# Kernel optimization log

Measured on AMD Instinct MI355X. Metric: run time of the kernel, lower is better.

The kernel has to match this reference:

```python
import jax, jax.numpy as jnp
import numpy as np

B, S, D = 2, 2048, 768          # batch, n_ctx, d_model
NQK, DQK = 12, 64               # n_qk_heads, d_qk_head
NOV, DOV = 768, 1               # n_ov_heads, d_ov_head
R = NOV // NQK                  # OV heads per QK head
VKV = 4                         # virtual_kv_num
BASE = 10000.0
SCALE = DQK ** 0.5              # cfg.attn_scale default


def _rotary_sin_cos():
    # TransformerLens-style (non-adjacent-pairs): freq repeated as (2 d)
    pos = jnp.arange(S, dtype=jnp.float32)
    freq = BASE ** (jnp.arange(0, DQK, 2, dtype=jnp.float32) / DQK)
    freq = jnp.concatenate([freq, freq])          # [DQK]
    angles = pos[:, None] / freq[None, :]         # [S, DQK]
    return jnp.sin(angles), jnp.cos(angles)


def _apply_rotary(x, sin, cos):
    # x: [b, pos, head, DQK]; rotary_dim == d_qk_head so full rotation
    half = DQK // 2
    rot = jnp.concatenate([-x[..., half:], x[..., :half]], axis=-1)
    return x * cos[None, :, None, :] + rot * sin[None, :, None, :]


def setup_inputs() -> dict:
    key = jax.random.key(0)
    ks = jax.random.split(key, 7)
    std_qk = (2.0 / (D * DQK)) ** 0.5   # kaiming fan_in (d_model*d_head)
    std_ov = (2.0 / (D * DOV)) ** 0.5
    std_o = (2.0 / (DOV * D)) ** 0.5
    sin, cos = _rotary_sin_cos()
    return {
        "resid": jax.random.normal(ks[0], (B, S, D), jnp.float32),
        "W_Q": jax.random.normal(ks[1], (NQK, D, DQK), jnp.float32) * std_qk,
        "W_K": jax.random.normal(ks[2], (NQK, D, DQK), jnp.float32) * std_qk,
        "W_V": jax.random.normal(ks[3], (NOV, D, DOV), jnp.float32) * std_ov,
        "W_O": jax.random.normal(ks[4], (NOV, DOV, D), jnp.float32) * std_o,
        "b_Q": jnp.zeros((NQK, DQK), jnp.float32),
        "b_K": jnp.zeros((NQK, DQK), jnp.float32),
        "b_V": jnp.zeros((NOV, DOV), jnp.float32),
        "virtual_k": jax.random.normal(ks[5], (VKV, NQK, DQK), jnp.float32) * (2.0 / (NQK * DQK)) ** 0.5,
        "virtual_v": jnp.zeros((VKV, NOV, DOV), jnp.float32),  # init zeros, requires_grad=False
        "rotary_sin": sin,
        "rotary_cos": cos,
    }


def reference(resid, W_Q, W_K, W_V, W_O, b_Q, b_K, b_V,
              virtual_k, virtual_v, rotary_sin, rotary_cos):
    # q/k/v projections: per-head low-rank maps + bias  -> [b, s, h, d]
    q = jnp.einsum('bsm,hmd->bshd', resid, W_Q) + b_Q
    k = jnp.einsum('bsm,hmd->bshd', resid, W_K) + b_K
    v = jnp.einsum('bsm,hmd->bshd', resid, W_V) + b_V
    # rotary on q and k
    q = _apply_rotary(q, rotary_sin, rotary_cos)
    k = _apply_rotary(k, rotary_sin, rotary_cos)
    # append virtual KV tokens at the end of the key axis
    k = jnp.concatenate([k, jnp.broadcast_to(virtual_k[None], (B, VKV, NQK, DQK))], axis=1)
    v = jnp.concatenate([v, jnp.broadcast_to(virtual_v[None], (B, VKV, NOV, DOV))], axis=1)
    # full attention scores [b, nqk, S, S+VKV]
    scores = jnp.einsum('bqhd,bkhd->bhqk', q, k) / SCALE
    # causal mask: tril(ones(S, S+VKV), diagonal=VKV) -> key j visible iff j <= i + VKV
    qi = jnp.arange(S)[:, None]
    kj = jnp.arange(S + VKV)[None, :]
    mask = kj <= qi + VKV
    scores = jnp.where(mask[None, None], scores, -jnp.inf)
    pattern = jax.nn.softmax(scores, axis=-1)
    pattern = jnp.where(jnp.isnan(pattern), 0.0, pattern)
    # group OV heads by QK head: v [b, k, NOV, DOV] -> [b, NQK, R, k, DOV]
    v_r = jnp.transpose(v, (0, 2, 1, 3)).reshape(B, NQK, R, S + VKV, DOV)
    z = jnp.einsum('bnqk,bnrkh->bnrqh', pattern, v_r)       # [b, NQK, R, S, DOV]
    z = z.reshape(B, NOV, S, DOV).transpose(0, 2, 1, 3)      # [b, S, NOV, DOV]
    out = jnp.einsum('bqhd,hdm->bqm', z, W_O)                # cal_out (no b_O)
    return out
```

## Files before the change

### kernel.cpp

```cpp
#include <hip/hip_runtime.h>

typedef __attribute__((ext_vector_type(8))) __bf16 bf16x8;
typedef __attribute__((ext_vector_type(4))) __bf16 bf16x4;
typedef __attribute__((ext_vector_type(4))) float  f32x4;

__device__ __forceinline__ void gld_lds16(const void* g, void* l) {
  __builtin_amdgcn_global_load_lds(
      (const __attribute__((address_space(1))) unsigned int*)g,
      (__attribute__((address_space(3))) unsigned int*)l, 16, 0, 0);
}


__global__ __launch_bounds__(256) void prep_kernel(
    const float* __restrict__ resid, const float* __restrict__ WQ,
    const float* __restrict__ WK, const float* __restrict__ WV,
    const float* __restrict__ WO,
    __bf16* __restrict__ Rb, __bf16* __restrict__ Wt1, __bf16* __restrict__ Wt2)
{
  int t = blockIdx.x * 256 + threadIdx.x;
  if (t < 786432) {
    f32x4 v = *(const f32x4*)(resid + (size_t)t * 4);
    bf16x4 o;
#pragma unroll
    for (int j = 0; j < 4; ++j) o[j] = (__bf16)v[j];
    *(bf16x4*)(Rb + (size_t)t * 4) = o;
    return;
  }
  t -= 786432;
  if (t < 1769472) {
    int nn = t / 768, k = t - nn * 768;
    float v;
    if (nn < 768)       v = WQ[(nn >> 6) * 49152 + k * 64 + (nn & 63)];
    else if (nn < 1536) v = WK[((nn - 768) >> 6) * 49152 + k * 64 + ((nn - 768) & 63)];
    else                v = WV[(nn - 1536) * 768 + k];
    Wt1[t] = (__bf16)v;
    return;
  }
  t -= 1769472;
  int nn = t / 768, k = t - nn * 768;
  Wt2[t] = (__bf16)WO[k * 768 + nn];
}

template<int OUTF>
__global__ __launch_bounds__(256) void gemm_bt(
    const __bf16* __restrict__ A, const __bf16* __restrict__ Bt,
    void* __restrict__ C, int M, int N, int K, int ldc)
{
  __shared__ __align__(16) char smem[65536];
  const int tid = threadIdx.x;
  const int l = tid & 63, wv = tid >> 6;
  const int wr = wv >> 1, wc = wv & 1;
  const int l15 = l & 15, lg = l >> 4;
  const int m0 = blockIdx.y * 128, n0 = blockIdx.x * 128;
  const int sw = (l15 & 7) << 4;

  auto stage = [&](int buf, int k0) {
    char* a_l = smem + buf * 32768;
    char* b_l = a_l + 16384;
#pragma unroll
    for (int c = 0; c < 4; ++c) {
      int i2 = c * 256 + tid;
      int row = i2 >> 3, slt = i2 & 7;
      gld_lds16(A + (size_t)(m0 + row) * K + k0 + ((slt ^ (row & 7)) * 8), a_l + i2 * 16);
    }
#pragma unroll
    for (int c = 0; c < 4; ++c) {
      int i2 = c * 256 + tid;
      int row = i2 >> 3, slt = i2 & 7;
      gld_lds16(Bt + (size_t)(n0 + row) * K + k0 + ((slt ^ (row & 7)) * 8), b_l + i2 * 16);
    }
  };

  f32x4 acc[4][4] = {};
  stage(0, 0);
  __syncthreads();
  int cur = 0;
  for (int k0 = 0; k0 < K; k0 += 64) {
    if (k0 + 64 < K) stage(cur ^ 1, k0 + 64);
    char* a_lds = smem + cur * 32768;
    char* b_lds = a_lds + 16384;
#pragma unroll
    for (int kk = 0; kk < 2; ++kk) {
      bf16x8 af[4], bfr[4];
#pragma unroll
      for (int i = 0; i < 4; ++i) {
        int mr = wr * 64 + i * 16 + l15;
        af[i]  = *(const bf16x8*)(a_lds + mr * 128 + ((lg * 16 + kk * 64) ^ sw));
        int nr = wc * 64 + i * 16 + l15;
        bfr[i] = *(const bf16x8*)(b_lds + nr * 128 + ((lg * 16 + kk * 64) ^ sw));
      }
#pragma unroll
      for (int i = 0; i < 4; ++i)
#pragma unroll
        for (int j = 0; j < 4; ++j)
          acc[i][j] = __builtin_amdgcn_mfma_f32_16x16x32_bf16(af[i], bfr[j], acc[i][j], 0, 0, 0);
    }
    __syncthreads();
    cur ^= 1;
  }
#pragma unroll
  for (int i = 0; i < 4; ++i)
#pragma unroll
    for (int j = 0; j < 4; ++j)
#pragma unroll
      for (int r = 0; r < 4; ++r) {
        int row = m0 + wr * 64 + i * 16 + lg * 4 + r;
        int col = n0 + wc * 64 + j * 16 + l15;
        if (OUTF) ((float*)C)[(size_t)row * ldc + col] = acc[i][j][r];
        else      ((__bf16*)C)[(size_t)row * ldc + col] = (__bf16)acc[i][j][r];
      }
}

__global__ __launch_bounds__(256) void qk_rotary(
    const __bf16* __restrict__ qkv, const float* __restrict__ bQ,
    const float* __restrict__ bK, const float* __restrict__ vk,
    const float* __restrict__ rsin, const float* __restrict__ rcos,
    __bf16* __restrict__ Qb, __bf16* __restrict__ Kb)
{
  int t = blockIdx.x * 256 + threadIdx.x;
  if (t < 196608) {
    int d0 = (t & 3) * 8;
    int x = t >> 2;
    int bh = x >> 11, s = x & 2047;
    int b = bh / 12, h = bh - b * 12;
    const __bf16* rowp = qkv + ((size_t)(b * 2048 + s)) * 2304 + h * 64;
    bf16x8 ql = *(const bf16x8*)(rowp + d0);
    bf16x8 qu = *(const bf16x8*)(rowp + d0 + 32);
    bf16x8 kl = *(const bf16x8*)(rowp + 768 + d0);
    bf16x8 ku = *(const bf16x8*)(rowp + 768 + d0 + 32);
    const float* bql = bQ + h * 64 + d0;
    const float* bkl = bK + h * 64 + d0;
    const float* snp = rsin + s * 64 + d0;
    const float* csp = rcos + s * 64 + d0;
    f32x4 bq0 = *(const f32x4*)(bql),      bq1 = *(const f32x4*)(bql + 4);
    f32x4 bq2 = *(const f32x4*)(bql + 32), bq3 = *(const f32x4*)(bql + 36);
    f32x4 bk0 = *(const f32x4*)(bkl),      bk1 = *(const f32x4*)(bkl + 4);
    f32x4 bk2 = *(const f32x4*)(bkl + 32), bk3 = *(const f32x4*)(bkl + 36);
    f32x4 sl0 = *(const f32x4*)(snp),      sl1 = *(const f32x4*)(snp + 4);
    f32x4 su0 = *(const f32x4*)(snp + 32), su1 = *(const f32x4*)(snp + 36);
    f32x4 cl0 = *(const f32x4*)(csp),      cl1 = *(const f32x4*)(csp + 4);
    f32x4 cu0 = *(const f32x4*)(csp + 32), cu1 = *(const f32x4*)(csp + 36);
    bf16x8 qlo, quo, klo, kuo;
#pragma unroll
    for (int j = 0; j < 8; ++j) {
      float snl = (j < 4) ? sl0[j & 3] : sl1[j & 3];
      float csl = (j < 4) ? cl0[j & 3] : cl1[j & 3];
      float snu = (j < 4) ? su0[j & 3] : su1[j & 3];
      float csu = (j < 4) ? cu0[j & 3] : cu1[j & 3];
      float q1 = (float)ql[j] + ((j < 4) ? bq0[j & 3] : bq1[j & 3]);
      float q2 = (float)qu[j] + ((j < 4) ? bq2[j & 3] : bq3[j & 3]);
      float k1 = (float)kl[j] + ((j < 4) ? bk0[j & 3] : bk1[j & 3]);
      float k2 = (float)ku[j] + ((j < 4) ? bk2[j & 3] : bk3[j & 3]);
      qlo[j] = (__bf16)((q1 * csl - q2 * snl) * 0.125f);
      quo[j] = (__bf16)((q2 * csu + q1 * snu) * 0.125f);
      klo[j] = (__bf16)(k1 * csl - k2 * snl);
      kuo[j] = (__bf16)(k2 * csu + k1 * snu);
    }
    __bf16* qb = Qb + ((size_t)bh * 2048 + s) * 64;
    __bf16* kb = Kb + ((size_t)bh * 2112 + s) * 64;
    *(bf16x8*)(qb + d0) = qlo;  *(bf16x8*)(qb + d0 + 32) = quo;
    *(bf16x8*)(kb + d0) = klo;  *(bf16x8*)(kb + d0 + 32) = kuo;
    return;
  }
  t -= 196608;
  if (t < 12288) {
    int d0 = (t & 7) * 8;
    int x = t >> 3;
    int bh = x >> 6, sp = x & 63;
    int h = bh % 12;
    bf16x8 o;
    if (sp < 4) {
      const float* vp = vk + ((size_t)sp * 12 + h) * 64 + d0;
      f32x4 v0 = *(const f32x4*)(vp), v1 = *(const f32x4*)(vp + 4);
#pragma unroll
      for (int j = 0; j < 8; ++j) o[j] = (__bf16)((j < 4) ? v0[j & 3] : v1[j & 3]);
    } else {
#pragma unroll
      for (int j = 0; j < 8; ++j) o[j] = (__bf16)0.0f;
    }
    *(bf16x8*)(Kb + ((size_t)bh * 2112 + 2048 + sp) * 64 + d0) = o;
  }
}

__global__ __launch_bounds__(256) void v_trans(
    const __bf16* __restrict__ qkv, const float* __restrict__ bV,
    const float* __restrict__ vv, __bf16* __restrict__ Vt)
{
  __shared__ float tile[64][65];
  int st = blockIdx.x, bh = blockIdx.y;
  int b = bh / 12, h = bh - b * 12;
  int tid = threadIdx.x;
#pragma unroll
  for (int c = 0; c < 2; ++c) {
    int chunk = c * 256 + tid;
    int srow = chunk >> 3, d0 = (chunk & 7) * 8;
    int s = st * 64 + srow;
    float vals[8];
    if (s < 2048) {
      bf16x8 v8 = *(const bf16x8*)(qkv + ((size_t)(b * 2048 + s)) * 2304 + 1536 + h * 64 + d0);
      const float* bvp = bV + h * 64 + d0;
      f32x4 b0 = *(const f32x4*)(bvp), b1 = *(const f32x4*)(bvp + 4);
#pragma unroll
      for (int j = 0; j < 8; ++j) vals[j] = (float)v8[j] + ((j < 4) ? b0[j & 3] : b1[j & 3]);
    } else if (s < 2052) {
      const float* vp = vv + (size_t)(s - 2048) * 768 + h * 64 + d0;
      f32x4 v0 = *(const f32x4*)(vp), v1 = *(const f32x4*)(vp + 4);
#pragma unroll
      for (int j = 0; j < 8; ++j) vals[j] = (j < 4) ? v0[j & 3] : v1[j & 3];
    } else {
#pragma unroll
      for (int j = 0; j < 8; ++j) vals[j] = 0.0f;
    }
#pragma unroll
    for (int j = 0; j < 8; ++j) tile[srow][d0 + j] = vals[j];
  }
  __syncthreads();
#pragma unroll
  for (int c = 0; c < 2; ++c) {
    int chunk = c * 256 + tid;
    int drow = chunk >> 3, s0 = (chunk & 7) * 8;
    bf16x8 o8;
#pragma unroll
    for (int j = 0; j < 8; ++j) o8[j] = (__bf16)tile[s0 + j][drow];
    *(bf16x8*)(Vt + ((size_t)bh * 64 + drow) * 2112 + st * 64 + s0) = o8;
  }
}

__global__ __launch_bounds__(256) void attn_kernel(
    const __bf16* __restrict__ Qb, const __bf16* __restrict__ Kb,
    const __bf16* __restrict__ Vt, __bf16* __restrict__ Z)
{
  __shared__ __align__(16) char smem[40960];
  char* p_lds = smem + 32768;
  const int tid = threadIdx.x;
  const int l = tid & 63, w = tid >> 6;
  const int l15 = l & 15, lg = l >> 4;
  const int idx = blockIdx.x;
  const int bh = idx % 24;
  const int qt = 31 - idx / 24;
  const int b = bh / 12, n = bh - b * 12;
  const int q16 = qt * 64 + w * 16;
  const int sw = (l15 & 7) << 4;
  const int qrow = w * 16 + l15;

  const __bf16* Kbase = Kb + (size_t)bh * 2112 * 64;
  const __bf16* Vbase = Vt + (size_t)bh * 64 * 2112;
  const int ntiles = qt + 2;

  auto stage = [&](int buf, int kt0) {
    char* k_l = smem + buf * 16384;
    char* v_l = k_l + 8192;
#pragma unroll
    for (int c = 0; c < 2; ++c) {
      int i2 = c * 256 + tid;
      int row = i2 >> 3, slt = i2 & 7;
      gld_lds16(Kbase + (kt0 + row) * 64 + ((slt ^ (row & 7)) * 8), k_l + i2 * 16);
    }
#pragma unroll
    for (int c = 0; c < 2; ++c) {
      int i2 = c * 256 + tid;
      int row = i2 >> 3, slt = i2 & 7;
      gld_lds16(Vbase + row * 2112 + kt0 + ((slt ^ (row & 7)) * 8), v_l + i2 * 16);
    }
  };

  stage(0, 0);

  const __bf16* qp = Qb + ((size_t)bh * 2048 + q16 + l15) * 64 + lg * 8;
  const bf16x8 qa0 = *(const bf16x8*)qp;
  const bf16x8 qa1 = *(const bf16x8*)(qp + 32);

  f32x4 o[4] = {};
  float mrun = -1e30f, lrun = 0.0f;
  __syncthreads();

  int cur = 0;
  for (int kt = 0; kt < ntiles; ++kt) {
    const int kt0 = kt * 64;
    if (kt + 1 < ntiles) stage(cur ^ 1, kt0 + 64);
    char* k_lds = smem + cur * 16384;
    char* v_lds = k_lds + 8192;

    if (kt0 <= q16 + 19) {
      f32x4 sfr[4];
#pragma unroll
      for (int kb = 0; kb < 4; ++kb) {
        int krow = kb * 16 + l15;
        f32x4 a = {};
        bf16x8 ka0 = *(const bf16x8*)(k_lds + krow * 128 + ((lg * 16) ^ sw));
        bf16x8 ka1 = *(const bf16x8*)(k_lds + krow * 128 + ((lg * 16 + 64) ^ sw));
        a = __builtin_amdgcn_mfma_f32_16x16x32_bf16(ka0, qa0, a, 0, 0, 0);
        a = __builtin_amdgcn_mfma_f32_16x16x32_bf16(ka1, qa1, a, 0, 0, 0);
        sfr[kb] = a;
      }
      if (kt >= qt) {
        int qlim = q16 + l15 + 4;
#pragma unroll
        for (int kb = 0; kb < 4; ++kb)
#pragma unroll
          for (int r = 0; r < 4; ++r) {
            int kg = kt0 + kb * 16 + lg * 4 + r;
            if (kg > qlim || kg >= 2052) sfr[kb][r] = -1e30f;
          }
      }
      float tmax = -1e30f;
#pragma unroll
      for (int kb = 0; kb < 4; ++kb)
#pragma unroll
        for (int r = 0; r < 4; ++r) tmax = fmaxf(tmax, sfr[kb][r]);
      tmax = fmaxf(tmax, __shfl_xor(tmax, 16));
      tmax = fmaxf(tmax, __shfl_xor(tmax, 32));
      float mnew = fmaxf(mrun, tmax);
      float fsc = __expf(mrun - mnew);
      float rsum = 0.0f;
#pragma unroll
      for (int kb = 0; kb < 4; ++kb) {
        bf16x4 pv;
#pragma unroll
        for (int r = 0; r < 4; ++r) {
          float p = __expf(sfr[kb][r] - mnew);
          rsum += p;
          pv[r] = (__bf16)p;
        }
        *(bf16x4*)(p_lds + qrow * 128 + ((kb * 32 + lg * 8) ^ sw)) = pv;
      }
      rsum += __shfl_xor(rsum, 16);
      rsum += __shfl_xor(rsum, 32);
      lrun = lrun * fsc + rsum;
      mrun = mnew;
      f32x4 fv;
#pragma unroll
      for (int r = 0; r < 4; ++r) fv[r] = __shfl(fsc, lg * 4 + r);
#pragma unroll
      for (int dv = 0; dv < 4; ++dv) o[dv] *= fv;
#pragma unroll
      for (int kblk = 0; kblk < 2; ++kblk) {
        bf16x8 pa = *(const bf16x8*)(p_lds + qrow * 128 + ((kblk * 64 + lg * 16) ^ sw));
#pragma unroll
        for (int dv = 0; dv < 4; ++dv) {
          int vrow = dv * 16 + l15;
          bf16x8 vb = *(const bf16x8*)(v_lds + vrow * 128 + ((kblk * 64 + lg * 16) ^ sw));
          o[dv] = __builtin_amdgcn_mfma_f32_16x16x32_bf16(pa, vb, o[dv], 0, 0, 0);
        }
      }
    }
    __syncthreads();
    cur ^= 1;
  }
  float linv = 1.0f / lrun;
  f32x4 lv;
#pragma unroll
  for (int r = 0; r < 4; ++r) lv[r] = __shfl(linv, lg * 4 + r);
  __bf16* zbase = Z + ((size_t)b * 2048 + q16) * 768 + n * 64;
#pragma unroll
  for (int dv = 0; dv < 4; ++dv)
#pragma unroll
    for (int r = 0; r < 4; ++r)
      zbase[(lg * 4 + r) * 768 + dv * 16 + l15] = (__bf16)(o[dv][r] * lv[r]);
}

extern "C" void kernel_launch(void* const* d_in, const int* in_sizes, int n_in,
                              void* d_out, int out_size, void* d_ws, size_t ws_size,
                              hipStream_t stream)
{
  const float* resid = (const float*)d_in[0];
  const float* WQ   = (const float*)d_in[1];
  const float* WK   = (const float*)d_in[2];
  const float* WV   = (const float*)d_in[3];
  const float* WO   = (const float*)d_in[4];
  const float* bQ   = (const float*)d_in[5];
  const float* bK   = (const float*)d_in[6];
  const float* bV   = (const float*)d_in[7];
  const float* vk   = (const float*)d_in[8];
  const float* vv   = (const float*)d_in[9];
  const float* rsin = (const float*)d_in[10];
  const float* rcos = (const float*)d_in[11];

  char* ws = (char*)d_ws;
  __bf16* Rb  = (__bf16*)(ws);
  __bf16* Wt1 = (__bf16*)(ws + 6291456);
  __bf16* Wt2 = (__bf16*)(ws + 9830400);
  __bf16* QKV = (__bf16*)(ws + 11010048);
  __bf16* Qb  = (__bf16*)(ws + 29884416);
  __bf16* Kb  = (__bf16*)(ws + 36175872);
  __bf16* Vt  = (__bf16*)(ws + 42663936);
  __bf16* Zb  = (__bf16*)(ws + 49152000);

  prep_kernel<<<12288, 256, 0, stream>>>(resid, WQ, WK, WV, WO, Rb, Wt1, Wt2);
  gemm_bt<0><<<dim3(18, 32), 256, 0, stream>>>(Rb, Wt1, (void*)QKV, 4096, 2304, 768, 2304);
  qk_rotary<<<816, 256, 0, stream>>>(QKV, bQ, bK, vk, rsin, rcos, Qb, Kb);
  v_trans<<<dim3(33, 24), 256, 0, stream>>>(QKV, bV, vv, Vt);
  attn_kernel<<<768, 256, 0, stream>>>(Qb, Kb, Vt, Zb);
  gemm_bt<1><<<dim3(6, 32), 256, 0, stream>>>(Zb, Wt2, d_out, 4096, 768, 768, 768);
}
```

Measured before the change: 189.6 us.

## Split attention over key chunks with merge kernel, tile weight transposes, tune GEMM

Splits the causal attention along the key axis into chunks of up to eight tiles, writing unnormalized partial outputs plus max/sum, then merges them in a new kernel; this balances the triangular workload and raises block count. Weight transposes for WQ/WK/WO move to an LDS-tiled kernel for coalesced access, and the output projection uses a narrower 64-column tile for more blocks. Softmax uses exp2 with log2e folded into the Q scale and skips the accumulator rescale when no row max changed. Adds an extra kernel launch and partial-result traffic.

```diff
diff --git a/kernel.cpp b/kernel.cpp
--- a/kernel.cpp
+++ b/kernel.cpp
@@ -10,12 +10,11 @@
       (__attribute__((address_space(3))) unsigned int*)l, 16, 0, 0);
 }
 
+#define QSCALE 0.18033688011112042f
 
 __global__ __launch_bounds__(256) void prep_kernel(
-    const float* __restrict__ resid, const float* __restrict__ WQ,
-    const float* __restrict__ WK, const float* __restrict__ WV,
-    const float* __restrict__ WO,
-    __bf16* __restrict__ Rb, __bf16* __restrict__ Wt1, __bf16* __restrict__ Wt2)
+    const float* __restrict__ resid, const float* __restrict__ WV,
+    __bf16* __restrict__ Rb, __bf16* __restrict__ Wt1)
 {
   int t = blockIdx.x * 256 + threadIdx.x;
   if (t < 786432) {
@@ -27,35 +26,78 @@
     return;
   }
   t -= 786432;
-  if (t < 1769472) {
-    int nn = t / 768, k = t - nn * 768;
-    float v;
-    if (nn < 768)       v = WQ[(nn >> 6) * 49152 + k * 64 + (nn & 63)];
-    else if (nn < 1536) v = WK[((nn - 768) >> 6) * 49152 + k * 64 + ((nn - 768) & 63)];
-    else                v = WV[(nn - 1536) * 768 + k];
-    Wt1[t] = (__bf16)v;
-    return;
-  }
-  t -= 1769472;
-  int nn = t / 768, k = t - nn * 768;
-  Wt2[t] = (__bf16)WO[k * 768 + nn];
-}
-
-template<int OUTF>
+  if (t < 73728) {
+    const float* vp = WV + (size_t)t * 8;
+    f32x4 v0 = *(const f32x4*)vp, v1 = *(const f32x4*)(vp + 4);
+    bf16x8 o;
+#pragma unroll
+    for (int j = 0; j < 8; ++j) o[j] = (__bf16)((j < 4) ? v0[j & 3] : v1[j & 3]);
+    *(bf16x8*)(Wt1 + (size_t)1536 * 768 + (size_t)t * 8) = o;
+  }
+}
+
+__global__ __launch_bounds__(256) void wtrans_kernel(
+    const float* __restrict__ WQ, const float* __restrict__ WK,
+    const float* __restrict__ WO,
+    __bf16* __restrict__ Wt1, __bf16* __restrict__ Wt2)
+{
+  __shared__ float tile[64][65];
+  int g = blockIdx.x, tid = threadIdx.x;
+  const float* src; __bf16* dst;
+  int sld, dld, r0, c0, drow0, dcol0;
+  if (g < 288) {
+    const float* W = (g < 144) ? WQ : WK;
+    int gg = g % 144;
+    int h = gg / 12, kt = gg - h * 12;
+    src = W + (size_t)h * 49152; sld = 64; r0 = kt * 64; c0 = 0;
+    dst = Wt1; dld = 768;
+    drow0 = ((g < 144) ? 0 : 768) + h * 64; dcol0 = kt * 64;
+  } else {
+    int gg = g - 288;
+    int rt = gg / 12, ct = gg - rt * 12;
+    src = WO; sld = 768; r0 = rt * 64; c0 = ct * 64;
+    dst = Wt2; dld = 768; drow0 = ct * 64; dcol0 = rt * 64;
+  }
+#pragma unroll
+  for (int c = 0; c < 4; ++c) {
+    int li = c * 256 + tid;
+    int r = li >> 4, cc = (li & 15) * 4;
+    f32x4 v = *(const f32x4*)(src + (size_t)(r0 + r) * sld + c0 + cc);
+#pragma unroll
+    for (int j = 0; j < 4; ++j) tile[r][cc + j] = v[j];
+  }
+  __syncthreads();
+#pragma unroll
+  for (int c = 0; c < 2; ++c) {
+    int li = c * 256 + tid;
+    int cc = li >> 3, rr = (li & 7) * 8;
+    bf16x8 o;
+#pragma unroll
+    for (int j = 0; j < 8; ++j) o[j] = (__bf16)tile[rr + j][cc];
+    *(bf16x8*)(dst + (size_t)(drow0 + cc) * dld + dcol0 + rr) = o;
+  }
+}
+
+template<int OUTF, int BN>
 __global__ __launch_bounds__(256) void gemm_bt(
     const __bf16* __restrict__ A, const __bf16* __restrict__ Bt,
     void* __restrict__ C, int M, int N, int K, int ldc)
 {
-  __shared__ __align__(16) char smem[65536];
+  constexpr int LDSB = BN * 128;
+  constexpr int BUF  = 16384 + LDSB;
+  constexpr int BSTG = BN / 32;
+  constexpr int IM   = (BN == 128) ? 4 : 2;
+  __shared__ __align__(16) char smem[2 * BUF];
   const int tid = threadIdx.x;
   const int l = tid & 63, wv = tid >> 6;
-  const int wr = wv >> 1, wc = wv & 1;
   const int l15 = l & 15, lg = l >> 4;
-  const int m0 = blockIdx.y * 128, n0 = blockIdx.x * 128;
+  const int wmb = (BN == 128) ? (wv >> 1) * 64 : wv * 32;
+  const int wnb = (BN == 128) ? (wv & 1) * 64 : 0;
+  const int m0 = blockIdx.y * 128, n0 = blockIdx.x * BN;
   const int sw = (l15 & 7) << 4;
 
   auto stage = [&](int buf, int k0) {
-    char* a_l = smem + buf * 32768;
+    char* a_l = smem + buf * BUF;
     char* b_l = a_l + 16384;
 #pragma unroll
     for (int c = 0; c < 4; ++c) {
@@ -64,33 +106,36 @@
       gld_lds16(A + (size_t)(m0 + row) * K + k0 + ((slt ^ (row & 7)) * 8), a_l + i2 * 16);
     }
 #pragma unroll
-    for (int c = 0; c < 4; ++c) {
+    for (int c = 0; c < BSTG; ++c) {
       int i2 = c * 256 + tid;
       int row = i2 >> 3, slt = i2 & 7;
       gld_lds16(Bt + (size_t)(n0 + row) * K + k0 + ((slt ^ (row & 7)) * 8), b_l + i2 * 16);
     }
   };
 
-  f32x4 acc[4][4] = {};
+  f32x4 acc[IM][4] = {};
   stage(0, 0);
   __syncthreads();
   int cur = 0;
   for (int k0 = 0; k0 < K; k0 += 64) {
     if (k0 + 64 < K) stage(cur ^ 1, k0 + 64);
-    char* a_lds = smem + cur * 32768;
+    char* a_lds = smem + cur * BUF;
     char* b_lds = a_lds + 16384;
 #pragma unroll
     for (int kk = 0; kk < 2; ++kk) {
-      bf16x8 af[4], bfr[4];
-#pragma unroll
-      for (int i = 0; i < 4; ++i) {
-        int mr = wr * 64 + i * 16 + l15;
-        af[i]  = *(const bf16x8*)(a_lds + mr * 128 + ((lg * 16 + kk * 64) ^ sw));
-        int nr = wc * 64 + i * 16 + l15;
-        bfr[i] = *(const bf16x8*)(b_lds + nr * 128 + ((lg * 16 + kk * 64) ^ sw));
-      }
-#pragma unroll
-      for (int i = 0; i < 4; ++i)
+      bf16x8 af[IM], bfr[4];
+#pragma unroll
+      for (int i = 0; i < IM; ++i) {
+        int mr = wmb + i * 16 + l15;
+        af[i] = *(const bf16x8*)(a_lds + mr * 128 + ((lg * 16 + kk * 64) ^ sw));
+      }
+#pragma unroll
+      for (int j = 0; j < 4; ++j) {
+        int nr = wnb + j * 16 + l15;
+        bfr[j] = *(const bf16x8*)(b_lds + nr * 128 + ((lg * 16 + kk * 64) ^ sw));
+      }
+#pragma unroll
+      for (int i = 0; i < IM; ++i)
 #pragma unroll
         for (int j = 0; j < 4; ++j)
           acc[i][j] = __builtin_amdgcn_mfma_f32_16x16x32_bf16(af[i], bfr[j], acc[i][j], 0, 0, 0);
@@ -99,13 +144,13 @@
     cur ^= 1;
   }
 #pragma unroll
-  for (int i = 0; i < 4; ++i)
+  for (int i = 0; i < IM; ++i)
 #pragma unroll
     for (int j = 0; j < 4; ++j)
 #pragma unroll
       for (int r = 0; r < 4; ++r) {
-        int row = m0 + wr * 64 + i * 16 + lg * 4 + r;
-        int col = n0 + wc * 64 + j * 16 + l15;
+        int row = m0 + wmb + i * 16 + lg * 4 + r;
+        int col = n0 + wnb + j * 16 + l15;
         if (OUTF) ((float*)C)[(size_t)row * ldc + col] = acc[i][j][r];
         else      ((__bf16*)C)[(size_t)row * ldc + col] = (__bf16)acc[i][j][r];
       }
@@ -151,8 +196,8 @@
       float q2 = (float)qu[j] + ((j < 4) ? bq2[j & 3] : bq3[j & 3]);
       float k1 = (float)kl[j] + ((j < 4) ? bk0[j & 3] : bk1[j & 3]);
       float k2 = (float)ku[j] + ((j < 4) ? bk2[j & 3] : bk3[j & 3]);
-      qlo[j] = (__bf16)((q1 * csl - q2 * snl) * 0.125f);
-      quo[j] = (__bf16)((q2 * csu + q1 * snu) * 0.125f);
+      qlo[j] = (__bf16)((q1 * csl - q2 * snl) * QSCALE);
+      quo[j] = (__bf16)((q2 * csu + q1 * snu) * QSCALE);
       klo[j] = (__bf16)(k1 * csl - k2 * snl);
       kuo[j] = (__bf16)(k2 * csu + k1 * snu);
     }
@@ -228,7 +273,8 @@
 
 __global__ __launch_bounds__(256) void attn_kernel(
     const __bf16* __restrict__ Qb, const __bf16* __restrict__ Kb,
-    const __bf16* __restrict__ Vt, __bf16* __restrict__ Z)
+    const __bf16* __restrict__ Vt, __bf16* __restrict__ Opart,
+    float* __restrict__ ML)
 {
   __shared__ __align__(16) char smem[40960];
   char* p_lds = smem + 32768;
@@ -237,15 +283,18 @@
   const int l15 = l & 15, lg = l >> 4;
   const int idx = blockIdx.x;
   const int bh = idx % 24;
-  const int qt = 31 - idx / 24;
-  const int b = bh / 12, n = bh - b * 12;
+  int pidx = idx / 24;
+  int qt = 31, rem = pidx;
+  for (;;) { int c = (qt + 9) >> 3; if (rem < c) break; rem -= c; --qt; }
+  const int ts = rem * 8;
+  const int te = min(ts + 8, qt + 2);
+  const int slot = bh * 84 + pidx;
   const int q16 = qt * 64 + w * 16;
   const int sw = (l15 & 7) << 4;
   const int qrow = w * 16 + l15;
 
   const __bf16* Kbase = Kb + (size_t)bh * 2112 * 64;
   const __bf16* Vbase = Vt + (size_t)bh * 64 * 2112;
-  const int ntiles = qt + 2;
 
   auto stage = [&](int buf, int kt0) {
     char* k_l = smem + buf * 16384;
@@ -264,7 +313,7 @@
     }
   };
 
-  stage(0, 0);
+  stage(0, ts * 64);
 
   const __bf16* qp = Qb + ((size_t)bh * 2048 + q16 + l15) * 64 + lg * 8;
   const bf16x8 qa0 = *(const bf16x8*)qp;
@@ -275,9 +324,9 @@
   __syncthreads();
 
   int cur = 0;
-  for (int kt = 0; kt < ntiles; ++kt) {
+  for (int kt = ts; kt < te; ++kt) {
     const int kt0 = kt * 64;
-    if (kt + 1 < ntiles) stage(cur ^ 1, kt0 + 64);
+    if (kt + 1 < te) stage(cur ^ 1, kt0 + 64);
     char* k_lds = smem + cur * 16384;
     char* v_lds = k_lds + 8192;
 
@@ -311,14 +360,15 @@
       tmax = fmaxf(tmax, __shfl_xor(tmax, 16));
       tmax = fmaxf(tmax, __shfl_xor(tmax, 32));
       float mnew = fmaxf(mrun, tmax);
-      float fsc = __expf(mrun - mnew);
+      int needresc = __any(mnew > mrun);
+      float fsc = exp2f(mrun - mnew);
       float rsum = 0.0f;
 #pragma unroll
       for (int kb = 0; kb < 4; ++kb) {
         bf16x4 pv;
 #pragma unroll
         for (int r = 0; r < 4; ++r) {
-          float p = __expf(sfr[kb][r] - mnew);
+          float p = exp2f(sfr[kb][r] - mnew);
           rsum += p;
           pv[r] = (__bf16)p;
         }
@@ -328,11 +378,13 @@
       rsum += __shfl_xor(rsum, 32);
       lrun = lrun * fsc + rsum;
       mrun = mnew;
-      f32x4 fv;
-#pragma unroll
-      for (int r = 0; r < 4; ++r) fv[r] = __shfl(fsc, lg * 4 + r);
-#pragma unroll
-      for (int dv = 0; dv < 4; ++dv) o[dv] *= fv;
+      if (needresc) {
+        f32x4 fv;
+#pragma unroll
+        for (int r = 0; r < 4; ++r) fv[r] = __shfl(fsc, lg * 4 + r);
+#pragma unroll
+        for (int dv = 0; dv < 4; ++dv) o[dv] *= fv;
+      }
 #pragma unroll
       for (int kblk = 0; kblk < 2; ++kblk) {
         bf16x8 pa = *(const bf16x8*)(p_lds + qrow * 128 + ((kblk * 64 + lg * 16) ^ sw));
@@ -347,16 +399,59 @@
     __syncthreads();
     cur ^= 1;
   }
-  float linv = 1.0f / lrun;
-  f32x4 lv;
-#pragma unroll
-  for (int r = 0; r < 4; ++r) lv[r] = __shfl(linv, lg * 4 + r);
-  __bf16* zbase = Z + ((size_t)b * 2048 + q16) * 768 + n * 64;
+  if (lg == 0) {
+    ML[slot * 128 + qrow] = mrun;
+    ML[slot * 128 + 64 + qrow] = lrun;
+  }
+  __bf16* op = Opart + (size_t)slot * 4096;
 #pragma unroll
   for (int dv = 0; dv < 4; ++dv)
 #pragma unroll
     for (int r = 0; r < 4; ++r)
-      zbase[(lg * 4 + r) * 768 + dv * 16 + l15] = (__bf16)(o[dv][r] * lv[r]);
+      op[(w * 16 + lg * 4 + r) * 64 + dv * 16 + l15] = (__bf16)o[dv][r];
+}
+
+__global__ __launch_bounds__(256) void attn_merge(
+    const __bf16* __restrict__ Opart, const float* __restrict__ ML,
+    __bf16* __restrict__ Z)
+{
+  const int idx = blockIdx.x;
+  const int bh = idx % 24, qt = idx / 24;
+  const int b = bh / 12, n = bh - b * 12;
+  int pbase = 0;
+  for (int q2 = 31; q2 > qt; --q2) pbase += (q2 + 9) >> 3;
+  const int ns = (qt + 9) >> 3;
+  const int t = threadIdx.x;
+  const int q = t >> 2, c0 = (t & 3) * 16;
+
+  float M = -1e30f;
+  for (int s = 0; s < ns; ++s)
+    M = fmaxf(M, ML[(bh * 84 + pbase + s) * 128 + q]);
+  float L = 0.0f;
+  float acc[16] = {};
+  for (int s = 0; s < ns; ++s) {
+    int slot = bh * 84 + pbase + s;
+    float ms = ML[slot * 128 + q], ls = ML[slot * 128 + 64 + q];
+    float wgt = exp2f(ms - M);
+    L += ls * wgt;
+    const __bf16* op = Opart + (size_t)slot * 4096 + q * 64 + c0;
+    bf16x8 o0 = *(const bf16x8*)op, o1 = *(const bf16x8*)(op + 8);
+#pragma unroll
+    for (int j = 0; j < 8; ++j) {
+      acc[j]     += wgt * (float)o0[j];
+      acc[8 + j] += wgt * (float)o1[j];
+    }
+  }
+  float inv = 1.0f / L;
+  bf16x8 z0, z1;
+#pragma unroll
+  for (int j = 0; j < 8; ++j) {
+    z0[j] = (__bf16)(acc[j] * inv);
+    z1[j] = (__bf16)(acc[8 + j] * inv);
+  }
+  __bf16* zp = Z + ((size_t)(b * 2048 + qt * 64 + q)) * 768 + n * 64 + c0;
+  *(bf16x8*)zp = z0;
+  *(bf16x8*)(zp + 8) = z1;
 }
 
 extern "C" void kernel_launch(void* const* d_in, const int* in_sizes, int n_in,
@@ -385,11 +480,15 @@
   __bf16* Kb  = (__bf16*)(ws + 36175872);
   __bf16* Vt  = (__bf16*)(ws + 42663936);
   __bf16* Zb  = (__bf16*)(ws + 49152000);
-
-  prep_kernel<<<12288, 256, 0, stream>>>(resid, WQ, WK, WV, WO, Rb, Wt1, Wt2);
-  gemm_bt<0><<<dim3(18, 32), 256, 0, stream>>>(Rb, Wt1, (void*)QKV, 4096, 2304, 768, 2304);
+  __bf16* Opart = (__bf16*)(ws + 11010048);
+  float*  MLp   = (float*)(ws + 11010048 + 16515072);
+
+  prep_kernel<<<3360, 256, 0, stream>>>(resid, WV, Rb, Wt1);
+  wtrans_kernel<<<432, 256, 0, stream>>>(WQ, WK, WO, Wt1, Wt2);
+  gemm_bt<0, 128><<<dim3(18, 32), 256, 0, stream>>>(Rb, Wt1, (void*)QKV, 4096, 2304, 768, 2304);
   qk_rotary<<<816, 256, 0, stream>>>(QKV, bQ, bK, vk, rsin, rcos, Qb, Kb);
   v_trans<<<dim3(33, 24), 256, 0, stream>>>(QKV, bV, vv, Vt);
-  attn_kernel<<<768, 256, 0, stream>>>(Qb, Kb, Vt, Zb);
-  gemm_bt<1><<<dim3(6, 32), 256, 0, stream>>>(Zb, Wt2, d_out, 4096, 768, 768, 768);
-}
+  attn_kernel<<<2016, 256, 0, stream>>>(Qb, Kb, Vt, Opart, MLp);
+  attn_merge<<<768, 256, 0, stream>>>(Opart, MLp, Zb);
+  gemm_bt<1, 64><<<dim3(12, 32), 256, 0, stream>>>(Zb, Wt2, d_out, 4096, 768, 768, 768);
+}
```

Result: faster. 185.4 us (-2.2%).
